# Performance work log

Measured on AMD Instinct MI355X. Metric: run time of the kernel, lower is better.

The kernel has to match this reference:

```python
import jax, jax.numpy as jnp
import numpy as np

N, C, T, H, W = 4, 512, 8, 28, 28
CQ, CV = C // 8, C // 2  # 64, 256


def _maxpool222(a):
    # max_pool3d with kernel=stride=(2,2,2), VALID, over (t,h,w) of [n,c,t,h,w]
    return jax.lax.reduce_window(a, -jnp.inf, jax.lax.max,
                                 (1, 1, 2, 2, 2), (1, 1, 2, 2, 2), 'VALID')


def setup_inputs() -> dict:
    key = jax.random.key(0)
    ks = jax.random.split(key, 6)
    s = lambda fan_in: 1.0 / np.sqrt(fan_in)
    return {
        'x':  jax.random.normal(ks[0], (N, C, T, H, W), dtype=jnp.float32),
        'Wq': jax.random.normal(ks[1], (CQ, C), dtype=jnp.float32) * s(C),
        'Wk': jax.random.normal(ks[2], (CQ, C), dtype=jnp.float32) * s(C),
        'Wv': jax.random.normal(ks[3], (CV, C), dtype=jnp.float32) * s(C),
        'Wz': jax.random.normal(ks[4], (C, CV), dtype=jnp.float32) * s(CV),
        'y':  jax.random.normal(ks[5], (), dtype=jnp.float32) * 0.1,
    }


def reference(x, Wq, Wk, Wv, Wz, y):
    n, c, t, h, w = x.shape
    # 1x1x1 convs (no bias) = per-voxel channel mixing
    q = jnp.einsum('ncthw,oc->nothw', x, Wq)          # [n, CQ, t, h, w]
    k = _maxpool222(jnp.einsum('ncthw,oc->nothw', x, Wk))  # [n, CQ, t/2, h/2, w/2]
    v = _maxpool222(jnp.einsum('ncthw,oc->nothw', x, Wv))  # [n, CV, t/2, h/2, w/2]

    Lq = t * h * w
    Lk = k.shape[2] * k.shape[3] * k.shape[4]
    qf = q.reshape(n, q.shape[1], Lq)                 # [n, CQ, Lq]
    kf = k.reshape(n, k.shape[1], Lk)                 # [n, CQ, Lk]
    vf = v.reshape(n, v.shape[1], Lk)                 # [n, CV, Lk]

    # beta = softmax(q^T k) over kv axis (NOTE: no 1/sqrt(d) scaling, as in source)
    beta = jax.nn.softmax(jnp.einsum('ncq,nck->nqk', qf, kf), axis=-1)  # [n, Lq, Lk]
    att = jnp.einsum('nck,nqk->ncq', vf, beta)        # [n, CV, Lq]
    att = att.reshape(n, vf.shape[1], t, h, w)

    z = jnp.einsum('ncthw,oc->nothw', att, Wz)        # [n, C, t, h, w]
    return y * z + x
```

## Files before the change

kernel.cpp:

```cpp
#include <hip/hip_runtime.h>
#include <hip/hip_bf16.h>

#define LSP  6272
#define LK   784
#define CIN  512
#define CQo  64
#define CVo  256
#define NB   4

typedef __bf16  bf16x8 __attribute__((ext_vector_type(8)));
typedef __bf16  bf16x4 __attribute__((ext_vector_type(4)));
typedef float   f32x4  __attribute__((ext_vector_type(4)));

#define LDT  40

__global__ void wprep_kernel(const float* __restrict__ Wq, const float* __restrict__ Wk,
                             const float* __restrict__ Wv, const float* __restrict__ Wz,
                             __bf16* __restrict__ Wqkv, __bf16* __restrict__ Wzb)
{
    int idx = blockIdx.x * 256 + threadIdx.x;
    if (idx < 384 * 512) {
        int o = idx >> 9;
        float v = (o < 64) ? Wq[idx] : (o < 128) ? Wk[idx - 64 * 512] : Wv[idx - 128 * 512];
        Wqkv[idx] = (__bf16)v;
    }
    if (idx < 512 * 256) Wzb[idx] = (__bf16)Wz[idx];
}

__global__ __launch_bounds__(256) void qkv_gemm(const __bf16* __restrict__ Wqkv,
                                                const float* __restrict__ x,
                                                __bf16* __restrict__ qT,
                                                __bf16* __restrict__ kT,
                                                __bf16* __restrict__ vconv)
{
    __shared__ __attribute__((aligned(16))) __bf16 As[128 * LDT];
    __shared__ __attribute__((aligned(16))) __bf16 Bs[128 * LDT];
    int t = threadIdx.x;
    int p0 = blockIdx.x * 128;
    int m0 = blockIdx.y * 128;
    int n  = blockIdx.z;
    int lane = t & 63, wid = t >> 6;
    int wm = wid >> 1, wn = wid & 1;
    int lm = lane & 15, lk = lane >> 4;
    int cS = t >> 3, pqS = t & 7;

    f32x4 acc[4][4] = {};

    for (int kb = 0; kb < CIN; kb += 32) {
        #pragma unroll
        for (int i = 0; i < 2; i++) {
            int idx = i * 2048 + t * 8;
            int r = idx >> 5, k8 = idx & 31;
            *reinterpret_cast<uint4*>(&As[r * LDT + k8]) =
                *reinterpret_cast<const uint4*>(&Wqkv[(size_t)(m0 + r) * CIN + kb + k8]);
        }
        #pragma unroll
        for (int i = 0; i < 4; i++) {
            int p = i * 32 + pqS * 4;
            const float4 v = *reinterpret_cast<const float4*>(
                &x[((size_t)(n * CIN + kb + cS)) * LSP + p0 + p]);
            int csw = cS ^ ((pqS & 3) << 3);
            Bs[(p + 0) * LDT + csw] = (__bf16)v.x;
            Bs[(p + 1) * LDT + csw] = (__bf16)v.y;
            Bs[(p + 2) * LDT + csw] = (__bf16)v.z;
            Bs[(p + 3) * LDT + csw] = (__bf16)v.w;
        }
        __syncthreads();
        if (m0 == 0) {
            bf16x8 a[4], b[4];
            #pragma unroll
            for (int mi = 0; mi < 4; mi++)
                a[mi] = *reinterpret_cast<const bf16x8*>(&As[(wm * 64 + mi * 16 + lm) * LDT + lk * 8]);
            #pragma unroll
            for (int ni = 0; ni < 4; ni++) {
                int row = wn * 64 + ni * 16 + lm;
                b[ni] = *reinterpret_cast<const bf16x8*>(
                    &Bs[row * LDT + ((lk * 8) ^ (((row >> 2) & 3) << 3))]);
            }
            #pragma unroll
            for (int mi = 0; mi < 4; mi++)
                #pragma unroll
                for (int ni = 0; ni < 4; ni++)
                    acc[mi][ni] = __builtin_amdgcn_mfma_f32_16x16x32_bf16(a[mi], b[ni], acc[mi][ni], 0, 0, 0);
        } else {
            bf16x8 a[4], b[4];
            #pragma unroll
            for (int mi = 0; mi < 4; mi++) {
                int row = wn * 64 + mi * 16 + lm;
                a[mi] = *reinterpret_cast<const bf16x8*>(
                    &Bs[row * LDT + ((lk * 8) ^ (((row >> 2) & 3) << 3))]);
            }
            #pragma unroll
            for (int ni = 0; ni < 4; ni++)
                b[ni] = *reinterpret_cast<const bf16x8*>(&As[(wm * 64 + ni * 16 + lm) * LDT + lk * 8]);
            #pragma unroll
            for (int mi = 0; mi < 4; mi++)
                #pragma unroll
                for (int ni = 0; ni < 4; ni++)
                    acc[mi][ni] = __builtin_amdgcn_mfma_f32_16x16x32_bf16(a[mi], b[ni], acc[mi][ni], 0, 0, 0);
        }
        __syncthreads();
    }

    if (m0 == 0) {
        #pragma unroll
        for (int mi = 0; mi < 4; mi++) {
            int mloc = wm * 64 + mi * 16 + lk * 4;
            #pragma unroll
            for (int ni = 0; ni < 4; ni++) {
                int p = p0 + wn * 64 + ni * 16 + lm;
                bf16x4 o;
                o[0] = (__bf16)acc[mi][ni][0]; o[1] = (__bf16)acc[mi][ni][1];
                o[2] = (__bf16)acc[mi][ni][2]; o[3] = (__bf16)acc[mi][ni][3];
                if (mloc < 64)
                    *reinterpret_cast<bf16x4*>(&qT[((size_t)(n * LSP + p)) * 64 + mloc]) = o;
                else
                    *reinterpret_cast<bf16x4*>(&kT[((size_t)(n * LSP + p)) * 64 + (mloc - 64)]) = o;
            }
        }
    } else {
        #pragma unroll
        for (int mi = 0; mi < 4; mi++) {
            int p = p0 + wn * 64 + mi * 16 + lk * 4;
            #pragma unroll
            for (int ni = 0; ni < 4; ni++) {
                int cv = (m0 - 128) + wm * 64 + ni * 16 + lm;
                bf16x4 o;
                o[0] = (__bf16)acc[mi][ni][0]; o[1] = (__bf16)acc[mi][ni][1];
                o[2] = (__bf16)acc[mi][ni][2]; o[3] = (__bf16)acc[mi][ni][3];
                *reinterpret_cast<bf16x4*>(&vconv[((size_t)(n * CVo + cv)) * LSP + p]) = o;
            }
        }
    }
}

__global__ __launch_bounds__(256) void poolk_kernel(const __bf16* __restrict__ kT,
                                                    __bf16* __restrict__ kpT)
{
    int wid = threadIdx.x >> 6, lane = threadIdx.x & 63;
    int row = blockIdx.x * 4 + wid;
    int n = row / LK, pk = row % LK;
    int tp = pk / 196, rem = pk % 196, hp = rem / 14, wp = rem % 14;
    const __bf16* b = kT + ((size_t)n * LSP + tp * 2 * 784 + hp * 2 * 28 + wp * 2) * 64 + lane;
    float m =        (float)b[0];
    m = fmaxf(m, (float)b[64]);
    m = fmaxf(m, (float)b[28 * 64]);
    m = fmaxf(m, (float)b[29 * 64]);
    m = fmaxf(m, (float)b[784 * 64]);
    m = fmaxf(m, (float)b[785 * 64]);
    m = fmaxf(m, (float)b[812 * 64]);
    m = fmaxf(m, (float)b[813 * 64]);
    kpT[(size_t)row * 64 + lane] = (__bf16)m;
}

__global__ void poolv_kernel(const __bf16* __restrict__ vconv, __bf16* __restrict__ vp)
{
    int id = blockIdx.x * 256 + threadIdx.x;
    if (id >= NB * CVo * LK) return;
    int nc = id / LK, pk = id % LK;
    int tp = pk / 196, rem = pk % 196, hp = rem / 14, wp = rem % 14;
    const __bf16* b = vconv + (size_t)nc * LSP + tp * 2 * 784 + hp * 2 * 28 + wp * 2;
    float m =        (float)b[0];
    m = fmaxf(m, (float)b[1]);   m = fmaxf(m, (float)b[28]);  m = fmaxf(m, (float)b[29]);
    m = fmaxf(m, (float)b[784]); m = fmaxf(m, (float)b[785]); m = fmaxf(m, (float)b[812]); m = fmaxf(m, (float)b[813]);
    vp[id] = (__bf16)m;
}

__global__ __launch_bounds__(512) void flash3_kernel(
    const __bf16* __restrict__ qT, const __bf16* __restrict__ kpT,
    const __bf16* __restrict__ vp, __bf16* __restrict__ attT)
{
    __shared__ __attribute__((aligned(16))) __bf16 Kbuf[2][64 * 64];
    __shared__ __attribute__((aligned(16))) __bf16 Ps[128 * 64];
    __shared__ float scs[128];
    __shared__ float invl[128];

    int t = threadIdx.x;
    int lane = t & 63, w = t >> 6;
    int lm = lane & 15, lk = lane >> 4;
    int q0 = blockIdx.x * 128;
    int n  = blockIdx.y;
    int swz = (lm & 7) << 3;

    const __bf16* kbase = kpT + (size_t)n * LK * 64;
    const __bf16* vbase = vp  + (size_t)n * CVo * LK;

    bf16x8 qa[2];
    {
        const __bf16* qrow = &qT[((size_t)(n * LSP + q0 + w * 16 + lm)) * 64 + lk * 8];
        qa[0] = *reinterpret_cast<const bf16x8*>(qrow);
        qa[1] = *reinterpret_cast<const bf16x8*>(qrow + 32);
    }

    int kr = t >> 3, kc = t & 7;
    int kds = kr * 64 + ((kc * 8) ^ ((kr & 7) << 3));
    const __bf16* kgsrc = &kbase[(size_t)kr * 64 + kc * 8];

    const __bf16* vsrc[2][2];
    #pragma unroll
    for (int mi = 0; mi < 2; mi++)
        #pragma unroll
        for (int ks = 0; ks < 2; ks++)
            vsrc[mi][ks] = &vbase[(size_t)(w * 32 + mi * 16 + lm) * LK + ks * 32 + lk * 8];

    uint4 kreg;
    bf16x8 vcur[2][2], vnxt[2][2];

    kreg = *reinterpret_cast<const uint4*>(kgsrc);
    #pragma unroll
    for (int mi = 0; mi < 2; mi++)
        #pragma unroll
        for (int ks = 0; ks < 2; ks++)
            vcur[mi][ks] = *reinterpret_cast<const bf16x8*>(vsrc[mi][ks]);
    *reinterpret_cast<uint4*>(&Kbuf[0][kds]) = kreg;
    __syncthreads();

    f32x4 accO[2][8] = {};
    float m = -1e30f, l = 0.0f;
    int qrow = w * 16 + lm;

    for (int kt = 0; kt < 13; kt++) {
        int cur = kt & 1;
        bool have_next = (kt < 12);
        bool lastT = (kt == 12);
        if (have_next) {
            size_t off = (size_t)(kt + 1) * 64;
            kreg = *reinterpret_cast<const uint4*>(kgsrc + off * 64);
            #pragma unroll
            for (int mi = 0; mi < 2; mi++)
                #pragma unroll
                for (int ks = 0; ks < 2; ks++)
                    vnxt[mi][ks] = *reinterpret_cast<const bf16x8*>(vsrc[mi][ks] + off);
        }
        f32x4 accS[4] = {};
        #pragma unroll
        for (int kg = 0; kg < 4; kg++) {
            if (!lastT || kg == 0) {
                #pragma unroll
                for (int ks = 0; ks < 2; ks++) {
                    bf16x8 kf = *reinterpret_cast<const bf16x8*>(
                        &Kbuf[cur][(kg * 16 + lm) * 64 + ((ks * 32 + lk * 8) ^ swz)]);
                    accS[kg] = __builtin_amdgcn_mfma_f32_16x16x32_bf16(kf, qa[ks], accS[kg], 0, 0, 0);
                }
            } else {
                accS[kg][0] = -1e30f; accS[kg][1] = -1e30f;
                accS[kg][2] = -1e30f; accS[kg][3] = -1e30f;
            }
        }
        float v = -1e30f;
        #pragma unroll
        for (int kg = 0; kg < 4; kg++)
            #pragma unroll
            for (int r = 0; r < 4; r++) v = fmaxf(v, accS[kg][r]);
        v = fmaxf(v, __shfl_xor(v, 16));
        v = fmaxf(v, __shfl_xor(v, 32));
        float sc_out = 1.0f;
        if (__any(v - m > 8.0f)) {
            float mn = fmaxf(m, v);
            sc_out = __expf(m - mn);
            l *= sc_out;
            m = mn;
        }
        float lt = 0.0f;
        #pragma unroll
        for (int kg = 0; kg < 4; kg++) {
            bf16x4 pw;
            #pragma unroll
            for (int r = 0; r < 4; r++) {
                float p = __expf(accS[kg][r] - m);
                lt += p;
                pw[r] = (__bf16)p;
            }
            *reinterpret_cast<bf16x4*>(&Ps[qrow * 64 + ((kg * 16 + lk * 4) ^ swz)]) = pw;
        }
        lt += __shfl_xor(lt, 16);
        lt += __shfl_xor(lt, 32);
        l += lt;
        if (lk == 0) scs[qrow] = sc_out;
        __syncthreads();
        float s[8];
        #pragma unroll
        for (int ni = 0; ni < 8; ni++) s[ni] = scs[ni * 16 + lm];
        bool need = false;
        #pragma unroll
        for (int ni = 0; ni < 8; ni++) need = need || (s[ni] != 1.0f);
        if (__any(need)) {
            #pragma unroll
            for (int mi = 0; mi < 2; mi++)
                #pragma unroll
                for (int ni = 0; ni < 8; ni++)
                    #pragma unroll
                    for (int r = 0; r < 4; r++) accO[mi][ni][r] *= s[ni];
        }
        #pragma unroll
        for (int ks = 0; ks < 2; ks++) {
            bf16x8 pf[8];
            #pragma unroll
            for (int ni = 0; ni < 8; ni++)
                pf[ni] = *reinterpret_cast<const bf16x8*>(
                    &Ps[(ni * 16 + lm) * 64 + ((ks * 32 + lk * 8) ^ swz)]);
            #pragma unroll
            for (int mi = 0; mi < 2; mi++)
                #pragma unroll
                for (int ni = 0; ni < 8; ni++)
                    accO[mi][ni] = __builtin_amdgcn_mfma_f32_16x16x32_bf16(
                        vcur[mi][ks], pf[ni], accO[mi][ni], 0, 0, 0);
        }
        if (have_next)
            *reinterpret_cast<uint4*>(&Kbuf[cur ^ 1][kds]) = kreg;
        __syncthreads();
        #pragma unroll
        for (int mi = 0; mi < 2; mi++)
            #pragma unroll
            for (int ks = 0; ks < 2; ks++)
                vcur[mi][ks] = vnxt[mi][ks];
    }
    if (lk == 0) invl[qrow] = 1.0f / l;
    __syncthreads();
    #pragma unroll
    for (int ni = 0; ni < 8; ni++) {
        float inv = invl[ni * 16 + lm];
        __bf16* orow = &attT[((size_t)(n * LSP + q0 + ni * 16 + lm)) * CVo + w * 32 + lk * 4];
        #pragma unroll
        for (int mi = 0; mi < 2; mi++) {
            bf16x4 o;
            o[0] = (__bf16)(accO[mi][ni][0] * inv);
            o[1] = (__bf16)(accO[mi][ni][1] * inv);
            o[2] = (__bf16)(accO[mi][ni][2] * inv);
            o[3] = (__bf16)(accO[mi][ni][3] * inv);
            *reinterpret_cast<bf16x4*>(&orow[mi * 16]) = o;
        }
    }
}

__global__ __launch_bounds__(256) void z_gemm(const __bf16* __restrict__ Wzb,
                                              const __bf16* __restrict__ attT,
                                              const float* __restrict__ x,
                                              const float* __restrict__ yp,
                                              float* __restrict__ out)
{
    __shared__ __attribute__((aligned(16))) __bf16 As[128 * LDT];
    __shared__ __attribute__((aligned(16))) __bf16 Bs[128 * LDT];
    int t = threadIdx.x;
    int p0 = blockIdx.x * 128;
    int c0 = blockIdx.y * 128;
    int n  = blockIdx.z;
    int lane = t & 63, wid = t >> 6;
    int wm = wid >> 1, wn = wid & 1;
    int lm = lane & 15, lk = lane >> 4;

    f32x4 acc[4][4] = {};

    for (int kb = 0; kb < CVo; kb += 32) {
        #pragma unroll
        for (int i = 0; i < 2; i++) {
            int idx = i * 2048 + t * 8;
            int r = idx >> 5, k8 = idx & 31;
            *reinterpret_cast<uint4*>(&As[r * LDT + k8]) =
                *reinterpret_cast<const uint4*>(&attT[((size_t)(n * LSP + p0 + r)) * CVo + kb + k8]);
            *reinterpret_cast<uint4*>(&Bs[r * LDT + k8]) =
                *reinterpret_cast<const uint4*>(&Wzb[(size_t)(c0 + r) * CVo + kb + k8]);
        }
        __syncthreads();
        bf16x8 a[4], b[4];
        #pragma unroll
        for (int mi = 0; mi < 4; mi++)
            a[mi] = *reinterpret_cast<const bf16x8*>(&As[(wm * 64 + mi * 16 + lm) * LDT + lk * 8]);
        #pragma unroll
        for (int ni = 0; ni < 4; ni++)
            b[ni] = *reinterpret_cast<const bf16x8*>(&Bs[(wn * 64 + ni * 16 + lm) * LDT + lk * 8]);
        #pragma unroll
        for (int mi = 0; mi < 4; mi++)
            #pragma unroll
            for (int ni = 0; ni < 4; ni++)
                acc[mi][ni] = __builtin_amdgcn_mfma_f32_16x16x32_bf16(a[mi], b[ni], acc[mi][ni], 0, 0, 0);
        __syncthreads();
    }

    float yv = yp[0];
    #pragma unroll
    for (int mi = 0; mi < 4; mi++) {
        int p = p0 + wm * 64 + mi * 16 + lk * 4;
        #pragma unroll
        for (int ni = 0; ni < 4; ni++) {
            int c = c0 + wn * 64 + ni * 16 + lm;
            size_t o = ((size_t)(n * CIN + c)) * LSP + p;
            const float4 xv = *reinterpret_cast<const float4*>(&x[o]);
            float4 ov;
            ov.x = yv * acc[mi][ni][0] + xv.x;
            ov.y = yv * acc[mi][ni][1] + xv.y;
            ov.z = yv * acc[mi][ni][2] + xv.z;
            ov.w = yv * acc[mi][ni][3] + xv.w;
            *reinterpret_cast<float4*>(&out[o]) = ov;
        }
    }
}

extern "C" void kernel_launch(void* const* d_in, const int* in_sizes, int n_in,
                              void* d_out, int out_size, void* d_ws, size_t ws_size,
                              hipStream_t stream)
{
    const float* x  = (const float*)d_in[0];
    const float* Wq = (const float*)d_in[1];
    const float* Wk = (const float*)d_in[2];
    const float* Wv = (const float*)d_in[3];
    const float* Wz = (const float*)d_in[4];
    const float* y  = (const float*)d_in[5];
    float* out = (float*)d_out;
    __bf16* ws = (__bf16*)d_ws;

    __bf16* kT    = ws;
    __bf16* vconv = ws + (size_t)1605632;
    __bf16* qT    = ws + (size_t)8028160;
    __bf16* kpT   = ws + (size_t)9633792;
    __bf16* vp    = ws + (size_t)9834496;
    __bf16* attT  = ws + (size_t)10637312;
    __bf16* Wqkv  = ws + (size_t)17059840;
    __bf16* Wzb   = ws + (size_t)17256448;

    wprep_kernel  <<<dim3(768), 256, 0, stream>>>(Wq, Wk, Wv, Wz, Wqkv, Wzb);
    qkv_gemm      <<<dim3(49, 3, 4), 256, 0, stream>>>(Wqkv, x, qT, kT, vconv);
    poolk_kernel  <<<dim3(784), 256, 0, stream>>>(kT, kpT);
    poolv_kernel  <<<dim3(3136), 256, 0, stream>>>(vconv, vp);
    flash3_kernel <<<dim3(49, 4), 512, 0, stream>>>(qT, kpT, vp, attT);
    z_gemm        <<<dim3(49, 4, 4), 256, 0, stream>>>(Wzb, attT, x, y, out);
}
```

Baseline: 216.1 us.

## Pre-transpose x to bf16 and double-buffer LDS tiles in both GEMMs

Adds a kernel that converts x to a bf16 [n, p, c] transposed layout once, so the QKV GEMM can load tiles with 16-byte vector copies instead of doing per-element convert-and-scatter stores into LDS. Both the QKV and Z GEMMs now use double-buffered shared memory with register prefetch of the next K-slice, which overlaps global loads with MFMA work. The cost is an extra kernel launch, an extra read of x plus a write and re-read of a 25 MB bf16 copy, and twice the LDS per block.

New measurement: 210.8 us. 2.5% less time.

```diff
diff --git a/kernel.cpp b/kernel.cpp
--- a/kernel.cpp
+++ b/kernel.cpp
@@ -14,6 +14,35 @@
 
 #define LDT  40
 
+__global__ __launch_bounds__(256) void xt_kernel(const float* __restrict__ x,
+                                                 __bf16* __restrict__ xT)
+{
+    __shared__ __attribute__((aligned(16))) __bf16 tile[64][68];
+    int t = threadIdx.x;
+    int p0 = blockIdx.x * 64, c0 = blockIdx.y * 64, n = blockIdx.z;
+    #pragma unroll
+    for (int i = 0; i < 4; i++) {
+        int idx = i * 256 + t;
+        int c = idx >> 4, p4 = (idx & 15) * 4;
+        const float4 v = *reinterpret_cast<const float4*>(
+            &x[((size_t)(n * CIN + c0 + c)) * LSP + p0 + p4]);
+        tile[p4 + 0][c] = (__bf16)v.x;
+        tile[p4 + 1][c] = (__bf16)v.y;
+        tile[p4 + 2][c] = (__bf16)v.z;
+        tile[p4 + 3][c] = (__bf16)v.w;
+    }
+    __syncthreads();
+    #pragma unroll
+    for (int i = 0; i < 4; i++) {
+        int idx = i * 256 + t;
+        int p = idx >> 4, c4 = (idx & 15) * 4;
+        bf16x4 o;
+        o[0] = tile[p][c4 + 0]; o[1] = tile[p][c4 + 1];
+        o[2] = tile[p][c4 + 2]; o[3] = tile[p][c4 + 3];
+        *reinterpret_cast<bf16x4*>(&xT[((size_t)(n * LSP + p0 + p)) * CIN + c0 + c4]) = o;
+    }
+}
+
 __global__ void wprep_kernel(const float* __restrict__ Wq, const float* __restrict__ Wk,
                              const float* __restrict__ Wv, const float* __restrict__ Wz,
                              __bf16* __restrict__ Wqkv, __bf16* __restrict__ Wzb)
@@ -28,13 +57,13 @@
 }
 
 __global__ __launch_bounds__(256) void qkv_gemm(const __bf16* __restrict__ Wqkv,
-                                                const float* __restrict__ x,
+                                                const __bf16* __restrict__ xT,
                                                 __bf16* __restrict__ qT,
                                                 __bf16* __restrict__ kT,
                                                 __bf16* __restrict__ vconv)
 {
-    __shared__ __attribute__((aligned(16))) __bf16 As[128 * LDT];
-    __shared__ __attribute__((aligned(16))) __bf16 Bs[128 * LDT];
+    __shared__ __attribute__((aligned(16))) __bf16 As[2][128 * LDT];
+    __shared__ __attribute__((aligned(16))) __bf16 Bs[2][128 * LDT];
     int t = threadIdx.x;
     int p0 = blockIdx.x * 128;
     int m0 = blockIdx.y * 128;
@@ -42,62 +71,59 @@
     int lane = t & 63, wid = t >> 6;
     int wm = wid >> 1, wn = wid & 1;
     int lm = lane & 15, lk = lane >> 4;
-    int cS = t >> 3, pqS = t & 7;
-
+
+    const __bf16* wsrc = &Wqkv[(size_t)(m0 + (t >> 2)) * CIN + (t & 3) * 8];
+    const __bf16* xsrc = &xT[((size_t)(n * LSP + p0 + (t >> 2))) * CIN + (t & 3) * 8];
+    int dsoff = (t >> 2) * LDT + (t & 3) * 8;
+
+    uint4 wa[2], xb[2];
     f32x4 acc[4][4] = {};
 
-    for (int kb = 0; kb < CIN; kb += 32) {
-        #pragma unroll
-        for (int i = 0; i < 2; i++) {
-            int idx = i * 2048 + t * 8;
-            int r = idx >> 5, k8 = idx & 31;
-            *reinterpret_cast<uint4*>(&As[r * LDT + k8]) =
-                *reinterpret_cast<const uint4*>(&Wqkv[(size_t)(m0 + r) * CIN + kb + k8]);
-        }
-        #pragma unroll
-        for (int i = 0; i < 4; i++) {
-            int p = i * 32 + pqS * 4;
-            const float4 v = *reinterpret_cast<const float4*>(
-                &x[((size_t)(n * CIN + kb + cS)) * LSP + p0 + p]);
-            int csw = cS ^ ((pqS & 3) << 3);
-            Bs[(p + 0) * LDT + csw] = (__bf16)v.x;
-            Bs[(p + 1) * LDT + csw] = (__bf16)v.y;
-            Bs[(p + 2) * LDT + csw] = (__bf16)v.z;
-            Bs[(p + 3) * LDT + csw] = (__bf16)v.w;
-        }
-        __syncthreads();
+    wa[0] = *reinterpret_cast<const uint4*>(wsrc);
+    wa[1] = *reinterpret_cast<const uint4*>(wsrc + 64 * CIN);
+    xb[0] = *reinterpret_cast<const uint4*>(xsrc);
+    xb[1] = *reinterpret_cast<const uint4*>(xsrc + 64 * CIN);
+    *reinterpret_cast<uint4*>(&As[0][dsoff]) = wa[0];
+    *reinterpret_cast<uint4*>(&As[0][dsoff + 64 * LDT]) = wa[1];
+    *reinterpret_cast<uint4*>(&Bs[0][dsoff]) = xb[0];
+    *reinterpret_cast<uint4*>(&Bs[0][dsoff + 64 * LDT]) = xb[1];
+    __syncthreads();
+
+    for (int kt = 0; kt < 16; kt++) {
+        int cur = kt & 1;
+        if (kt < 15) {
+            int ko = (kt + 1) * 32;
+            wa[0] = *reinterpret_cast<const uint4*>(wsrc + ko);
+            wa[1] = *reinterpret_cast<const uint4*>(wsrc + 64 * CIN + ko);
+            xb[0] = *reinterpret_cast<const uint4*>(xsrc + ko);
+            xb[1] = *reinterpret_cast<const uint4*>(xsrc + 64 * CIN + ko);
+        }
+        bf16x8 a[4], b[4];
         if (m0 == 0) {
-            bf16x8 a[4], b[4];
             #pragma unroll
             for (int mi = 0; mi < 4; mi++)
-                a[mi] = *reinterpret_cast<const bf16x8*>(&As[(wm * 64 + mi * 16 + lm) * LDT + lk * 8]);
-            #pragma unroll
-            for (int ni = 0; ni < 4; ni++) {
-                int row = wn * 64 + ni * 16 + lm;
-                b[ni] = *reinterpret_cast<const bf16x8*>(
-                    &Bs[row * LDT + ((lk * 8) ^ (((row >> 2) & 3) << 3))]);
-            }
+                a[mi] = *reinterpret_cast<const bf16x8*>(&As[cur][(wm * 64 + mi * 16 + lm) * LDT + lk * 8]);
+            #pragma unroll
+            for (int ni = 0; ni < 4; ni++)
+                b[ni] = *reinterpret_cast<const bf16x8*>(&Bs[cur][(wn * 64 + ni * 16 + lm) * LDT + lk * 8]);
+        } else {
             #pragma unroll
             for (int mi = 0; mi < 4; mi++)
-                #pragma unroll
-                for (int ni = 0; ni < 4; ni++)
-                    acc[mi][ni] = __builtin_amdgcn_mfma_f32_16x16x32_bf16(a[mi], b[ni], acc[mi][ni], 0, 0, 0);
-        } else {
-            bf16x8 a[4], b[4];
-            #pragma unroll
-            for (int mi = 0; mi < 4; mi++) {
-                int row = wn * 64 + mi * 16 + lm;
-                a[mi] = *reinterpret_cast<const bf16x8*>(
-                    &Bs[row * LDT + ((lk * 8) ^ (((row >> 2) & 3) << 3))]);
-            }
+                a[mi] = *reinterpret_cast<const bf16x8*>(&Bs[cur][(wn * 64 + mi * 16 + lm) * LDT + lk * 8]);
             #pragma unroll
             for (int ni = 0; ni < 4; ni++)
-                b[ni] = *reinterpret_cast<const bf16x8*>(&As[(wm * 64 + ni * 16 + lm) * LDT + lk * 8]);
-            #pragma unroll
-            for (int mi = 0; mi < 4; mi++)
-                #pragma unroll
-                for (int ni = 0; ni < 4; ni++)
-                    acc[mi][ni] = __builtin_amdgcn_mfma_f32_16x16x32_bf16(a[mi], b[ni], acc[mi][ni], 0, 0, 0);
+                b[ni] = *reinterpret_cast<const bf16x8*>(&As[cur][(wm * 64 + ni * 16 + lm) * LDT + lk * 8]);
+        }
+        #pragma unroll
+        for (int mi = 0; mi < 4; mi++)
+            #pragma unroll
+            for (int ni = 0; ni < 4; ni++)
+                acc[mi][ni] = __builtin_amdgcn_mfma_f32_16x16x32_bf16(a[mi], b[ni], acc[mi][ni], 0, 0, 0);
+        if (kt < 15) {
+            *reinterpret_cast<uint4*>(&As[cur ^ 1][dsoff]) = wa[0];
+            *reinterpret_cast<uint4*>(&As[cur ^ 1][dsoff + 64 * LDT]) = wa[1];
+            *reinterpret_cast<uint4*>(&Bs[cur ^ 1][dsoff]) = xb[0];
+            *reinterpret_cast<uint4*>(&Bs[cur ^ 1][dsoff + 64 * LDT]) = xb[1];
         }
         __syncthreads();
     }
@@ -339,8 +365,8 @@
                                               const float* __restrict__ yp,
                                               float* __restrict__ out)
 {
-    __shared__ __attribute__((aligned(16))) __bf16 As[128 * LDT];
-    __shared__ __attribute__((aligned(16))) __bf16 Bs[128 * LDT];
+    __shared__ __attribute__((aligned(16))) __bf16 As[2][128 * LDT];
+    __shared__ __attribute__((aligned(16))) __bf16 Bs[2][128 * LDT];
     int t = threadIdx.x;
     int p0 = blockIdx.x * 128;
     int c0 = blockIdx.y * 128;
@@ -349,31 +375,50 @@
     int wm = wid >> 1, wn = wid & 1;
     int lm = lane & 15, lk = lane >> 4;
 
+    const __bf16* asrc = &attT[((size_t)(n * LSP + p0 + (t >> 2))) * CVo + (t & 3) * 8];
+    const __bf16* bsrc = &Wzb[(size_t)(c0 + (t >> 2)) * CVo + (t & 3) * 8];
+    int dsoff = (t >> 2) * LDT + (t & 3) * 8;
+
+    uint4 aa[2], bb[2];
     f32x4 acc[4][4] = {};
 
-    for (int kb = 0; kb < CVo; kb += 32) {
-        #pragma unroll
-        for (int i = 0; i < 2; i++) {
-            int idx = i * 2048 + t * 8;
-            int r = idx >> 5, k8 = idx & 31;
-            *reinterpret_cast<uint4*>(&As[r * LDT + k8]) =
-                *reinterpret_cast<const uint4*>(&attT[((size_t)(n * LSP + p0 + r)) * CVo + kb + k8]);
-            *reinterpret_cast<uint4*>(&Bs[r * LDT + k8]) =
-                *reinterpret_cast<const uint4*>(&Wzb[(size_t)(c0 + r) * CVo + kb + k8]);
-        }
-        __syncthreads();
+    aa[0] = *reinterpret_cast<const uint4*>(asrc);
+    aa[1] = *reinterpret_cast<const uint4*>(asrc + 64 * CVo);
+    bb[0] = *reinterpret_cast<const uint4*>(bsrc);
+    bb[1] = *reinterpret_cast<const uint4*>(bsrc + 64 * CVo);
+    *reinterpret_cast<uint4*>(&As[0][dsoff]) = aa[0];
+    *reinterpret_cast<uint4*>(&As[0][dsoff + 64 * LDT]) = aa[1];
+    *reinterpret_cast<uint4*>(&Bs[0][dsoff]) = bb[0];
+    *reinterpret_cast<uint4*>(&Bs[0][dsoff + 64 * LDT]) = bb[1];
+    __syncthreads();
+
+    for (int kt = 0; kt < 8; kt++) {
+        int cur = kt & 1;
+        if (kt < 7) {
+            int ko = (kt + 1) * 32;
+            aa[0] = *reinterpret_cast<const uint4*>(asrc + ko);
+            aa[1] = *reinterpret_cast<const uint4*>(asrc + 64 * CVo + ko);
+            bb[0] = *reinterpret_cast<const uint4*>(bsrc + ko);
+            bb[1] = *reinterpret_cast<const uint4*>(bsrc + 64 * CVo + ko);
+        }
         bf16x8 a[4], b[4];
         #pragma unroll
         for (int mi = 0; mi < 4; mi++)
-            a[mi] = *reinterpret_cast<const bf16x8*>(&As[(wm * 64 + mi * 16 + lm) * LDT + lk * 8]);
+            a[mi] = *reinterpret_cast<const bf16x8*>(&As[cur][(wm * 64 + mi * 16 + lm) * LDT + lk * 8]);
         #pragma unroll
         for (int ni = 0; ni < 4; ni++)
-            b[ni] = *reinterpret_cast<const bf16x8*>(&Bs[(wn * 64 + ni * 16 + lm) * LDT + lk * 8]);
+            b[ni] = *reinterpret_cast<const bf16x8*>(&Bs[cur][(wn * 64 + ni * 16 + lm) * LDT + lk * 8]);
         #pragma unroll
         for (int mi = 0; mi < 4; mi++)
             #pragma unroll
             for (int ni = 0; ni < 4; ni++)
                 acc[mi][ni] = __builtin_amdgcn_mfma_f32_16x16x32_bf16(a[mi], b[ni], acc[mi][ni], 0, 0, 0);
+        if (kt < 7) {
+            *reinterpret_cast<uint4*>(&As[cur ^ 1][dsoff]) = aa[0];
+            *reinterpret_cast<uint4*>(&As[cur ^ 1][dsoff + 64 * LDT]) = aa[1];
+            *reinterpret_cast<uint4*>(&Bs[cur ^ 1][dsoff]) = bb[0];
+            *reinterpret_cast<uint4*>(&Bs[cur ^ 1][dsoff + 64 * LDT]) = bb[1];
+        }
         __syncthreads();
     }
 
@@ -409,17 +454,19 @@
     float* out = (float*)d_out;
     __bf16* ws = (__bf16*)d_ws;
 
-    __bf16* kT    = ws;
-    __bf16* vconv = ws + (size_t)1605632;
-    __bf16* qT    = ws + (size_t)8028160;
-    __bf16* kpT   = ws + (size_t)9633792;
-    __bf16* vp    = ws + (size_t)9834496;
-    __bf16* attT  = ws + (size_t)10637312;
-    __bf16* Wqkv  = ws + (size_t)17059840;
-    __bf16* Wzb   = ws + (size_t)17256448;
-
+    __bf16* xT    = ws;
+    __bf16* kT    = ws + (size_t)12845056;
+    __bf16* vconv = ws + (size_t)14450688;
+    __bf16* qT    = ws + (size_t)20873216;
+    __bf16* kpT   = ws + (size_t)22478848;
+    __bf16* vp    = ws + (size_t)22679552;
+    __bf16* attT  = ws + (size_t)23482368;
+    __bf16* Wqkv  = ws + (size_t)29904896;
+    __bf16* Wzb   = ws + (size_t)30101504;
+
+    xt_kernel     <<<dim3(98, 8, 4), 256, 0, stream>>>(x, xT);
     wprep_kernel  <<<dim3(768), 256, 0, stream>>>(Wq, Wk, Wv, Wz, Wqkv, Wzb);
-    qkv_gemm      <<<dim3(49, 3, 4), 256, 0, stream>>>(Wqkv, x, qT, kT, vconv);
+    qkv_gemm      <<<dim3(49, 3, 4), 256, 0, stream>>>(Wqkv, xT, qT, kT, vconv);
     poolk_kernel  <<<dim3(784), 256, 0, stream>>>(kT, kpT);
     poolv_kernel  <<<dim3(3136), 256, 0, stream>>>(vconv, vp);
     flash3_kernel <<<dim3(49, 4), 512, 0, stream>>>(qT, kpT, vp, attT);
```
